# Kernel optimization log

Measured on AMD Instinct MI355X. Metric: run time of the kernel, lower is better.

## Reference

```python
import jax, jax.numpy as jnp
import numpy as np

DIM = 128
K = 4
B, H, W = 2, 256, 256
DEFORM_WEIGHT = 0.3


def conv2d(x, w, b, pad):
    # x [B,C,H,W], w [O,I,kh,kw], stride 1
    y = jax.lax.conv_general_dilated(
        x, w, (1, 1), [(pad, pad), (pad, pad)],
        dimension_numbers=('NCHW', 'OIHW', 'NCHW'))
    return y + b[None, :, None, None]


def gelu(x):
    return jax.nn.gelu(x, approximate=False)  # torch nn.GELU default (erf)


def grid_sample_k(feat, grid):
    """Bilinear grid_sample, padding_mode='border', align_corners=True.
    feat: [B,C,H,W]; grid: [B,K,H,W,2] (x,y) in [-1,1]. Returns [B,C,K,H,W]."""
    Bn, C, Hh, Ww = feat.shape
    px = (grid[..., 0] + 1.0) * 0.5 * (Ww - 1)
    py = (grid[..., 1] + 1.0) * 0.5 * (Hh - 1)
    px = jnp.clip(px, 0.0, Ww - 1)
    py = jnp.clip(py, 0.0, Hh - 1)
    x0 = jnp.floor(px).astype(jnp.int32)
    y0 = jnp.floor(py).astype(jnp.int32)
    x1 = jnp.minimum(x0 + 1, Ww - 1)
    y1 = jnp.minimum(y0 + 1, Hh - 1)
    wx = (px - x0)[:, None]  # [B,1,K,H,W]
    wy = (py - y0)[:, None]
    featf = feat.reshape(Bn, C, Hh * Ww)

    def gather(yi, xi):
        idx = (yi * Ww + xi).reshape(Bn, -1)  # [B, K*H*W]
        g = jax.vmap(lambda f, i: f[:, i])(featf, idx)  # [B,C,K*H*W]
        return g.reshape(Bn, C, *yi.shape[1:])

    v00 = gather(y0, x0)
    v01 = gather(y0, x1)
    v10 = gather(y1, x0)
    v11 = gather(y1, x1)
    return (v00 * (1 - wx) * (1 - wy) + v01 * wx * (1 - wy)
            + v10 * (1 - wx) * wy + v11 * wx * wy)


def setup_inputs() -> dict:
    key = jax.random.key(0)
    ks = jax.random.split(key, 16)
    nrm = lambda k, shape, s: jax.random.normal(k, shape, dtype=jnp.float32) * s
    return {
        'query_feat': jax.random.normal(ks[0], (B, DIM, H, W), dtype=jnp.float32),
        'key_feat': jax.random.normal(ks[1], (B, DIM, H, W), dtype=jnp.float32),
        # offset_net: Conv(dim,dim,3) -> GELU -> Conv(dim,2K,3); small scale keeps offsets sane
        'ow1': nrm(ks[2], (DIM, DIM, 3, 3), 0.02), 'ob1': jnp.zeros((DIM,), jnp.float32),
        'ow2': nrm(ks[3], (2 * K, DIM, 3, 3), 0.01), 'ob2': jnp.zeros((2 * K,), jnp.float32),
        # weight_net: Conv(dim,dim//4,3) -> GELU -> Conv(dim//4,K,1)
        'ww1': nrm(ks[4], (DIM // 4, DIM, 3, 3), 0.05), 'wb1': jnp.zeros((DIM // 4,), jnp.float32),
        'ww2': nrm(ks[5], (K, DIM // 4, 1, 1), 0.05), 'wb2': jnp.zeros((K,), jnp.float32),
        # fusion_conv: Conv(dim,dim,1) -> GELU -> Conv(dim,dim,1)
        'fw1': nrm(ks[6], (DIM, DIM, 1, 1), 0.05), 'fb1': jnp.zeros((DIM,), jnp.float32),
        'fw2': nrm(ks[7], (DIM, DIM, 1, 1), 0.05), 'fb2': jnp.zeros((DIM,), jnp.float32),
    }


def reference(query_feat, key_feat, ow1, ob1, ow2, ob2, ww1, wb1, ww2, wb2,
              fw1, fb1, fw2, fb2):
    offsets = conv2d(gelu(conv2d(query_feat, ow1, ob1, 1)), ow2, ob2, 1)  # [B,2K,H,W]
    wlog = conv2d(gelu(conv2d(query_feat, ww1, wb1, 1)), ww2, wb2, 0)     # [B,K,H,W]
    Bn, C, Hh, Ww = key_feat.shape
    Kp = wlog.shape[1]
    off = offsets.reshape(Bn, Kp, 2, Hh, Ww).transpose(0, 1, 3, 4, 2)  # [B,K,H,W,2]
    gy, gx = jnp.meshgrid(jnp.linspace(-1.0, 1.0, Hh),
                          jnp.linspace(-1.0, 1.0, Ww), indexing='ij')
    base = jnp.stack([gx, gy], axis=-1).astype(off.dtype)  # [H,W,2] (x,y)
    scale = jnp.array([Ww / 2.0, Hh / 2.0], dtype=off.dtype)
    grid = jnp.clip(base + off / scale, -1.0, 1.0)  # [B,K,H,W,2]
    sampled = grid_sample_k(key_feat, grid)  # [B,C,K,H,W]
    wsoft = jax.nn.softmax(wlog, axis=1)[:, None]  # [B,1,K,H,W]
    agg = (sampled * wsoft).sum(axis=2)  # [B,C,H,W]
    fused = conv2d(gelu(conv2d(agg, fw1, fb1, 0)), fw2, fb2, 0)
    return query_feat + fused * DEFORM_WEIGHT
```

## Files before the change

kernel.cpp:

```cpp
#include <hip/hip_runtime.h>
#include <hip/hip_fp16.h>

typedef unsigned short u16;
typedef __attribute__((ext_vector_type(8))) short bf16x8;
typedef __attribute__((ext_vector_type(4))) float f32x4;

constexpr int B_ = 2, C_ = 128, H_ = 256, W_ = 256, P_ = H_ * W_;
constexpr int HP_ = 258, WP_ = 258;

union HU { __half2 h; unsigned int u; };

__device__ __forceinline__ float bf2f(u16 u) {
  union { unsigned int i; float f; } v; v.i = ((unsigned int)u) << 16; return v.f;
}
__device__ __forceinline__ u16 f2bf(float f) {
  union { float f; unsigned int i; } v; v.f = f;
  return (u16)((v.i + 0x7fffu + ((v.i >> 16) & 1u)) >> 16);
}
__device__ __forceinline__ float gelu_f(float x) {
  float u = x * (1.5957691216057308f + 0.071354816272f * x * x);
  return x / (1.0f + __expf(-u));
}

__device__ __forceinline__ void async16(const u16* g, u16* l) {
  __builtin_amdgcn_global_load_lds(
      (const __attribute__((address_space(1))) unsigned int*)g,
      (__attribute__((address_space(3))) unsigned int*)l, 16, 0, 0);
}

__global__ __launch_bounds__(256) void prologue(
    const float* __restrict__ q, const float* __restrict__ key,
    const float* __restrict__ ow1, const float* __restrict__ ow2,
    const float* __restrict__ ww1, const float* __restrict__ fw1,
    const float* __restrict__ fw2,
    u16* __restrict__ qpad, u16* __restrict__ keyn, u16* __restrict__ t1pad,
    u16* __restrict__ wb) {
  __shared__ u16 l[64 * 66];
  const int id = blockIdx.x, tid = threadIdx.x;
  if (id < 8192) {
    int z = id >> 10, r = id & 1023;
    int bx = r & 3, by = r >> 2;
    const float* in; u16* out; int OW, opad;
    if (z < 4) { in = q; out = qpad; OW = WP_; opad = 1; }
    else { z -= 4; in = key; out = keyn; OW = W_; opad = 0; }
    int b = z >> 1, c0 = (z & 1) * 64;
    int h = by, w0 = bx * 64;
    for (int it = 0; it < 4; ++it) {
      int lin = it * 256 + tid;
      int c = lin >> 4, w4 = (lin & 15) * 4;
      float4 v = *(const float4*)&in[(((size_t)b * C_ + c0 + c) * H_ + h) * W_ + w0 + w4];
      l[c * 66 + w4 + 0] = f2bf(v.x);
      l[c * 66 + w4 + 1] = f2bf(v.y);
      l[c * 66 + w4 + 2] = f2bf(v.z);
      l[c * 66 + w4 + 3] = f2bf(v.w);
    }
    __syncthreads();
    int OH = (opad ? HP_ : H_);
    for (int it = 0; it < 16; ++it) {
      int lin = it * 256 + tid;
      int w = lin >> 6, c = lin & 63;
      out[(((size_t)b * OH + h + opad) * OW + (w0 + w + opad)) * C_ + c0 + c] = l[c * 66 + w];
    }
  } else if (id < 10256) {
    int j = id - 8192;
    u16* buf = (j < 1032) ? qpad : t1pad;
    int idx = ((j < 1032) ? j : j - 1032) * 256 + tid;
    int c = idx & 127;
    int t = idx >> 7;
    int pos = t % 258;
    int side = (t / 258) & 3;
    int b = t / (258 * 4);
    int h, w;
    if (side == 0) { h = 0; w = pos; }
    else if (side == 1) { h = 257; w = pos; }
    else if (side == 2) { h = pos; w = 0; }
    else { h = pos; w = 257; }
    buf[(((size_t)b * HP_ + h) * WP_ + w) * C_ + c] = 0;
  } else {
    int idx = (id - 10256) * 256 + tid;
    float v;
    if (idx < 184320) {
      int e = idx & 7, lr = (idx >> 3) & 15, kb = (idx >> 7) & 3;
      int t = idx >> 9;
      int g = t % 10, u = t / 10;
      int cq = u & 3, tap = u >> 2;
      int ci = cq * 32 + kb * 8 + e, co = g * 16 + lr;
      v = (co < 128) ? ow1[(co * 128 + ci) * 9 + tap]
                     : ww1[((co - 128) * 128 + ci) * 9 + tap];
    } else if (idx < 202752) {
      int j = idx - 184320;
      int e = j & 7, lr = (j >> 3) & 15, kb = (j >> 7) & 3;
      int cq = (j >> 9) & 3, tap = j >> 11;
      int ci = cq * 32 + kb * 8 + e, co = lr;
      v = (co < 8) ? ow2[(co * 128 + ci) * 9 + tap] : 0.0f;
    } else if (idx < 219136) {
      v = fw1[idx - 202752];
    } else {
      v = fw2[idx - 219136];
    }
    wb[idx] = f2bf(v);
  }
}

__global__ __launch_bounds__(512, 4) void conv3_big(
    const u16* __restrict__ A, const u16* __restrict__ Wf,
    const float* __restrict__ bias1, const float* __restrict__ bias2,
    u16* __restrict__ outb, u16* __restrict__ outw) {
  constexpr int RPX = 36, ROWU = RPX * 32;
  __shared__ __align__(16) u16 As[6 * ROWU];
  const int tid = threadIdx.x, lane = tid & 63, wave = tid >> 6;
  const int id = blockIdx.x;
  const int s = id >> 3;
  const int h0 = (((id & 7) << 3) | (s & 7)) << 2;
  const int w0 = ((s >> 3) & 7) << 5;
  const int b = s >> 6;
  const int wr = wave >> 1, wc = wave & 1;
  const int wn = wc * 80;
  const int lr = lane & 15, kq = lane >> 4;
  const int gbase = wn >> 4;

  int preA[2][3];
#pragma unroll
  for (int i = 0; i < 2; i++)
#pragma unroll
    for (int kx = 0; kx < 3; kx++) {
      int pxv = i * 16 + lr + kx;
      preA[i][kx] = (pxv * 4 + (kq ^ ((pxv >> 1) & 3))) * 8;
    }

  f32x4 acc[2][5];
#pragma unroll
  for (int i = 0; i < 2; i++)
#pragma unroll
    for (int j = 0; j < 5; j++) { f32x4 z = {0.f, 0.f, 0.f, 0.f}; acc[i][j] = z; }

  for (int cq = 0; cq < 4; ++cq) {
    const int ci0 = cq * 32;
    __syncthreads();
    for (int i = tid; i < 864; i += 512) {
      int ry = i / 144;
      int rem = i - ry * 144;
      int px = rem >> 2, c8 = rem & 3;
      int g = c8 ^ ((px >> 1) & 3);
      async16(A + ((size_t)(b * HP_ + h0 + ry) * WP_ + (w0 + px)) * 128 + ci0 + g * 8,
              As + i * 8);
    }
    __syncthreads();
#pragma unroll
    for (int tap = 0; tap < 9; ++tap) {
      const int ky = tap / 3, kx = tap % 3;
      bf16x8 bfr[5], af[2];
#pragma unroll
      for (int j = 0; j < 5; ++j)
        bfr[j] = *(const bf16x8*)&Wf[(size_t)((((tap * 4 + cq) * 10 + gbase + j) * 4 + kq) * 16 + lr) * 8];
#pragma unroll
      for (int i = 0; i < 2; ++i)
        af[i] = *(const bf16x8*)&As[(wr + ky) * ROWU + preA[i][kx]];
#pragma unroll
      for (int i = 0; i < 2; i++)
#pragma unroll
        for (int j = 0; j < 5; j++)
          acc[i][j] = __builtin_amdgcn_mfma_f32_16x16x32_bf16(af[i], bfr[j], acc[i][j], 0, 0, 0);
    }
  }

  const int h = h0 + wr;
#pragma unroll
  for (int i = 0; i < 2; i++) {
#pragma unroll
    for (int j = 0; j < 5; j++) {
      const int co = wn + j * 16 + lr;
#pragma unroll
      for (int r = 0; r < 4; r++) {
        const int w = w0 + i * 16 + kq * 4 + r;
        float v = acc[i][j][r];
        if (co < 128) {
          v = gelu_f(v + bias1[co]);
          outb[(((size_t)b * HP_ + h + 1) * WP_ + (w + 1)) * 128 + co] = f2bf(v);
        } else {
          v = gelu_f(v + bias2[co - 128]);
          outw[((size_t)b * P_ + (size_t)h * W_ + w) * 32 + (co - 128)] = f2bf(v);
        }
      }
    }
  }
}

__global__ __launch_bounds__(256) void conv_off(
    const u16* __restrict__ A, const u16* __restrict__ Wf,
    const float* __restrict__ bias,
    const u16* __restrict__ w1b, const float* __restrict__ ww2,
    const float* __restrict__ wb2, uint4* __restrict__ desc) {
  constexpr int RPX = 66, ROWU = RPX * 32;
  __shared__ __align__(16) u16 As[6 * ROWU];
  float* off_lds = (float*)As;
  const int tid = threadIdx.x, lane = tid & 63, wave = tid >> 6;
  const int id = blockIdx.x;
  const int s = id >> 3;
  const int h0 = (((id & 7) << 3) | (s & 7)) << 2;
  const int w0 = ((s >> 3) & 3) << 6;
  const int b = s >> 5;
  const int lr = lane & 15, kq = lane >> 4;

  int preA[4][3];
#pragma unroll
  for (int i = 0; i < 4; i++)
#pragma unroll
    for (int kx = 0; kx < 3; kx++) {
      int pxv = i * 16 + lr + kx;
      preA[i][kx] = (pxv * 4 + (kq ^ ((pxv >> 1) & 3))) * 8;
    }

  f32x4 acc[4];
#pragma unroll
  for (int i = 0; i < 4; i++) { f32x4 z = {0.f, 0.f, 0.f, 0.f}; acc[i] = z; }

  for (int cq = 0; cq < 4; ++cq) {
    const int ci0 = cq * 32;
    __syncthreads();
    for (int i = tid; i < 1584; i += 256) {
      int ry = i / 264;
      int rem = i - ry * 264;
      int px = rem >> 2, c8 = rem & 3;
      int g = c8 ^ ((px >> 1) & 3);
      async16(A + ((size_t)(b * HP_ + h0 + ry) * WP_ + (w0 + px)) * 128 + ci0 + g * 8,
              As + i * 8);
    }
    __syncthreads();
#pragma unroll
    for (int tap = 0; tap < 9; ++tap) {
      const int ky = tap / 3, kx = tap % 3;
      bf16x8 bw = *(const bf16x8*)&Wf[(size_t)(((tap * 4 + cq) * 4 + kq) * 16 + lr) * 8];
      bf16x8 af[4];
#pragma unroll
      for (int i = 0; i < 4; ++i)
        af[i] = *(const bf16x8*)&As[(wave + ky) * ROWU + preA[i][kx]];
#pragma unroll
      for (int i = 0; i < 4; i++)
        acc[i] = __builtin_amdgcn_mfma_f32_16x16x32_bf16(af[i], bw, acc[i], 0, 0, 0);
    }
  }

  __syncthreads();
#pragma unroll
  for (int i = 0; i < 4; i++) {
#pragma unroll
    for (int r = 0; r < 4; r++) {
      if (lr < 8) {
        int px = i * 16 + (lane >> 4) * 4 + r;
        off_lds[(wave * 64 + px) * 9 + lr] = acc[i][r] + bias[lr];
      }
    }
  }
  __syncthreads();

  const int pp = tid;
  const int h = h0 + (pp >> 6), w = w0 + (pp & 63);
  const int pix = b * P_ + h * W_ + w;
  const u16* wp = w1b + (size_t)pix * 32;
  float f[32];
#pragma unroll
  for (int i = 0; i < 32; i += 2) {
    unsigned u = *(const unsigned*)&wp[i];
    f[i] = bf2f((u16)u); f[i + 1] = bf2f((u16)(u >> 16));
  }
  float lg[4];
#pragma unroll
  for (int k = 0; k < 4; k++) {
    float sacc = wb2[k];
#pragma unroll
    for (int i = 0; i < 32; i++) sacc = fmaf(ww2[k * 32 + i], f[i], sacc);
    lg[k] = sacc;
  }
  float mx = fmaxf(fmaxf(lg[0], lg[1]), fmaxf(lg[2], lg[3]));
  float e[4], sum = 0.f;
#pragma unroll
  for (int k = 0; k < 4; k++) { e[k] = __expf(lg[k] - mx); sum += e[k]; }
  const float inv = 1.0f / sum;
#pragma unroll
  for (int k = 0; k < 4; k++) {
    float ox = off_lds[pp * 9 + 2 * k], oy = off_lds[pp * 9 + 2 * k + 1];
    float gx = (2.0f * w / 255.0f - 1.0f) + ox * (1.0f / 128.0f);
    float gy = (2.0f * h / 255.0f - 1.0f) + oy * (1.0f / 128.0f);
    gx = fminf(fmaxf(gx, -1.f), 1.f);
    gy = fminf(fmaxf(gy, -1.f), 1.f);
    float px = fminf(fmaxf((gx + 1.f) * 127.5f, 0.f), 255.f);
    float py = fminf(fmaxf((gy + 1.f) * 127.5f, 0.f), 255.f);
    int x0 = (int)px, y0 = (int)py;
    int x1 = min(x0 + 1, 255), y1 = min(y0 + 1, 255);
    float wx = px - x0, wy = py - y0;
    float wk = e[k] * inv;
    float w00 = (1.f - wx) * (1.f - wy) * wk, w01 = wx * (1.f - wy) * wk;
    float w10 = (1.f - wx) * wy * wk,         w11 = wx * wy * wk;
    HU t01, t23;
    t01.h = __floats2half2_rn(w00, w01);
    t23.h = __floats2half2_rn(w10, w11);
    uint4 d;
    d.x = (unsigned)(y0 * 256 + x0) | ((unsigned)(x1 - x0) << 16) | ((unsigned)(y1 - y0) << 17);
    d.y = t01.u; d.z = t23.u; d.w = 0;
    desc[(size_t)pix * 4 + k] = d;
  }
}

__global__ __launch_bounds__(256) void sampler(
    const uint4* __restrict__ desc, const u16* __restrict__ keyn, u16* __restrict__ agg) {
  const int tid = threadIdx.x, lane = tid & 63, wv = tid >> 6;
  const int pix = blockIdx.x * 4 + wv;
  const int b = pix >> 16;
  const u16* kb = keyn + (size_t)b * (P_ * C_) + 2 * lane;
  float a0 = 0.f, a1 = 0.f;
#pragma unroll
  for (int k = 0; k < 4; ++k) {
    uint4 d = desc[(size_t)pix * 4 + k];
    const int boff = (int)(d.x & 0xFFFFu) << 7;
    const int o01 = (int)((d.x >> 16) & 1u) << 7;
    const int o10 = (int)((d.x >> 17) & 1u) << 15;
    const u16* c0 = kb + boff;
    unsigned u00 = *(const unsigned*)(c0);
    unsigned u01 = *(const unsigned*)(c0 + o01);
    unsigned u10 = *(const unsigned*)(c0 + o10);
    unsigned u11 = *(const unsigned*)(c0 + o10 + o01);
    HU t01, t23; t01.u = d.y; t23.u = d.z;
    float2 wA = __half22float2(t01.h);
    float2 wB = __half22float2(t23.h);
    a0 = fmaf(wA.x, bf2f((u16)u00), a0);
    a0 = fmaf(wA.y, bf2f((u16)u01), a0);
    a0 = fmaf(wB.x, bf2f((u16)u10), a0);
    a0 = fmaf(wB.y, bf2f((u16)u11), a0);
    a1 = fmaf(wA.x, bf2f((u16)(u00 >> 16)), a1);
    a1 = fmaf(wA.y, bf2f((u16)(u01 >> 16)), a1);
    a1 = fmaf(wB.x, bf2f((u16)(u10 >> 16)), a1);
    a1 = fmaf(wB.y, bf2f((u16)(u11 >> 16)), a1);
  }
  unsigned outu = ((unsigned)f2bf(a1) << 16) | (unsigned)f2bf(a0);
  *(unsigned*)&agg[(size_t)pix * C_ + 2 * lane] = outu;
}

__global__ __launch_bounds__(512, 4) void conv_fuse(
    const u16* __restrict__ Aagg, const u16* __restrict__ W1, const u16* __restrict__ W2,
    const float* __restrict__ b1, const float* __restrict__ b2,
    const float* __restrict__ resid, float* __restrict__ out) {
  __shared__ __align__(16) u16 SM[16384];
  __shared__ __align__(16) u16 T2[128 * 136];
  u16* As = SM;
  u16* Bs = SM + 8192;
  const int tid = threadIdx.x, lane = tid & 63, wave = tid >> 6;
  const int h = blockIdx.y, w0 = blockIdx.x * 128;
  const int b = blockIdx.z;
  const int wr = wave >> 1, wc = wave & 1;
  const int wm = wr * 32, wn = wc * 64;
  const int lr = lane & 15, kq = lane >> 4;
  const int sw = lr & 7;

  f32x4 acc[2][4];
#pragma unroll
  for (int i = 0; i < 2; i++)
#pragma unroll
    for (int j = 0; j < 4; j++) { f32x4 z = {0.f, 0.f, 0.f, 0.f}; acc[i][j] = z; }

  for (int c = 0; c < 2; ++c) {
    const int ci0 = c << 6;
    const u16* Ab = Aagg + (((size_t)b * H_ + h) * W_ + w0) * 128 + ci0;
    const u16* Wb = W1 + ci0;
    __syncthreads();
    for (int i = tid; i < 128 * 8; i += 512) {
      int r = i >> 3, cb = i & 7;
      async16(Ab + r * 128 + ((cb ^ (r & 7)) << 3), As + i * 8);
    }
    for (int i = tid; i < 128 * 8; i += 512) {
      int r = i >> 3, cb = i & 7;
      async16(Wb + r * 128 + ((cb ^ (r & 7)) << 3), Bs + i * 8);
    }
    __syncthreads();
#pragma unroll
    for (int ks = 0; ks < 2; ++ks) {
      const int kb = ks * 4 + kq;
      bf16x8 af[2], bfr[4];
#pragma unroll
      for (int i = 0; i < 2; i++)
        af[i] = *(const bf16x8*)&As[(wm + i * 16 + lr) * 64 + ((kb ^ sw) << 3)];
#pragma unroll
      for (int j = 0; j < 4; j++)
        bfr[j] = *(const bf16x8*)&Bs[(wn + j * 16 + lr) * 64 + ((kb ^ sw) << 3)];
#pragma unroll
      for (int i = 0; i < 2; i++)
#pragma unroll
        for (int j = 0; j < 4; j++)
          acc[i][j] = __builtin_amdgcn_mfma_f32_16x16x32_bf16(af[i], bfr[j], acc[i][j], 0, 0, 0);
    }
  }

#pragma unroll
  for (int i = 0; i < 2; i++)
#pragma unroll
    for (int j = 0; j < 4; j++) {
      const int co = wn + j * 16 + lr;
#pragma unroll
      for (int r = 0; r < 4; r++) {
        const int px = wm + i * 16 + kq * 4 + r;
        T2[px * 136 + co] = f2bf(gelu_f(acc[i][j][r] + b1[co]));
      }
    }
  __syncthreads();
  for (int i = tid; i < 2048; i += 512) {
    int r = i >> 4, sl = i & 15;
    int g = sl ^ (r & 7);
    async16(W2 + r * 128 + g * 8, SM + i * 8);
  }
  __syncthreads();

#pragma unroll
  for (int i = 0; i < 2; i++)
#pragma unroll
    for (int j = 0; j < 4; j++) { f32x4 z = {0.f, 0.f, 0.f, 0.f}; acc[i][j] = z; }
#pragma unroll
  for (int ks = 0; ks < 4; ++ks) {
    const int kc = ks * 4 + kq;
    bf16x8 af[2], bfr[4];
#pragma unroll
    for (int i = 0; i < 2; i++)
      af[i] = *(const bf16x8*)&T2[(wm + i * 16 + lr) * 136 + kc * 8];
#pragma unroll
    for (int j = 0; j < 4; j++) {
      int rr = wn + j * 16 + lr;
      bfr[j] = *(const bf16x8*)&SM[rr * 128 + (kc ^ (rr & 7)) * 8];
    }
#pragma unroll
    for (int i = 0; i < 2; i++)
#pragma unroll
      for (int j = 0; j < 4; j++)
        acc[i][j] = __builtin_amdgcn_mfma_f32_16x16x32_bf16(af[i], bfr[j], acc[i][j], 0, 0, 0);
  }

#pragma unroll
  for (int i = 0; i < 2; i++) {
#pragma unroll
    for (int j = 0; j < 4; j++) {
      const int co = wn + j * 16 + lr;
      const int w = w0 + wm + i * 16 + kq * 4;
      size_t idx = ((size_t)b * 128 + co) * (size_t)P_ + (size_t)h * W_ + w;
      float4 rv = *(const float4*)&resid[idx];
      float bi = b2[co];
      float4 ov;
      ov.x = rv.x + 0.3f * (acc[i][j][0] + bi);
      ov.y = rv.y + 0.3f * (acc[i][j][1] + bi);
      ov.z = rv.z + 0.3f * (acc[i][j][2] + bi);
      ov.w = rv.w + 0.3f * (acc[i][j][3] + bi);
      *(float4*)&out[idx] = ov;
    }
  }
}

extern "C" void kernel_launch(void* const* d_in, const int* in_sizes, int n_in,
                              void* d_out, int out_size, void* d_ws, size_t ws_size,
                              hipStream_t stream) {
  (void)in_sizes; (void)n_in; (void)out_size; (void)ws_size;
  const float* q   = (const float*)d_in[0];
  const float* key = (const float*)d_in[1];
  const float* ow1 = (const float*)d_in[2];
  const float* ob1 = (const float*)d_in[3];
  const float* ow2 = (const float*)d_in[4];
  const float* ob2 = (const float*)d_in[5];
  const float* ww1 = (const float*)d_in[6];
  const float* wb1 = (const float*)d_in[7];
  const float* ww2 = (const float*)d_in[8];
  const float* wb2 = (const float*)d_in[9];
  const float* fw1 = (const float*)d_in[10];
  const float* fb1 = (const float*)d_in[11];
  const float* fw2 = (const float*)d_in[12];
  const float* fb2 = (const float*)d_in[13];
  float* out = (float*)d_out;
  char* ws = (char*)d_ws;

  u16* qpad  = (u16*)(ws);
  u16* t1pad = (u16*)(ws + 34080768);
  u16* keyn  = (u16*)(ws + 68161536);
  u16* w1b   = (u16*)(ws + 101715968);
  u16* wbuf  = (u16*)(ws + 110104576);
  uint4* desc = (uint4*)ws;
  u16* agg = t1pad;

  prologue<<<11176, 256, 0, stream>>>(q, key, ow1, ow2, ww1, fw1, fw2,
                                      qpad, keyn, t1pad, wbuf);
  conv3_big<<<1024, 512, 0, stream>>>(qpad, wbuf, ob1, wb1, t1pad, w1b);
  conv_off<<<512, 256, 0, stream>>>(t1pad, wbuf + 184320, ob2, w1b, ww2, wb2, desc);
  sampler<<<32768, 256, 0, stream>>>(desc, keyn, agg);
  conv_fuse<<<dim3(2, 256, 2), 512, 0, stream>>>(agg, wbuf + 202752, wbuf + 219136,
                                                 fb1, fb2, q, out);
}
```

Before: 357.0 us.

## Fuse bilinear sampler into the 1x1 conv fuse kernel via shared memory

Merges the separate sampler kernel into the fusion-conv kernel. Each workgroup gathers its 128 pixels' aggregated features straight into a swizzled LDS tile, which removes the global write and re-read of the agg tensor and one kernel launch. Shared memory buffers are reassigned: the W1 slice is staged in T2, and the W2 load now overlaps the GELU epilogue. The trade-off is that the gather runs inside a kernel with fewer blocks and limited occupancy, so latency hiding for the random key reads may be weaker.

```diff
diff --git a/kernel.cpp b/kernel.cpp
--- a/kernel.cpp
+++ b/kernel.cpp
@@ -302,48 +302,13 @@
   }
 }
 
-__global__ __launch_bounds__(256) void sampler(
-    const uint4* __restrict__ desc, const u16* __restrict__ keyn, u16* __restrict__ agg) {
-  const int tid = threadIdx.x, lane = tid & 63, wv = tid >> 6;
-  const int pix = blockIdx.x * 4 + wv;
-  const int b = pix >> 16;
-  const u16* kb = keyn + (size_t)b * (P_ * C_) + 2 * lane;
-  float a0 = 0.f, a1 = 0.f;
-#pragma unroll
-  for (int k = 0; k < 4; ++k) {
-    uint4 d = desc[(size_t)pix * 4 + k];
-    const int boff = (int)(d.x & 0xFFFFu) << 7;
-    const int o01 = (int)((d.x >> 16) & 1u) << 7;
-    const int o10 = (int)((d.x >> 17) & 1u) << 15;
-    const u16* c0 = kb + boff;
-    unsigned u00 = *(const unsigned*)(c0);
-    unsigned u01 = *(const unsigned*)(c0 + o01);
-    unsigned u10 = *(const unsigned*)(c0 + o10);
-    unsigned u11 = *(const unsigned*)(c0 + o10 + o01);
-    HU t01, t23; t01.u = d.y; t23.u = d.z;
-    float2 wA = __half22float2(t01.h);
-    float2 wB = __half22float2(t23.h);
-    a0 = fmaf(wA.x, bf2f((u16)u00), a0);
-    a0 = fmaf(wA.y, bf2f((u16)u01), a0);
-    a0 = fmaf(wB.x, bf2f((u16)u10), a0);
-    a0 = fmaf(wB.y, bf2f((u16)u11), a0);
-    a1 = fmaf(wA.x, bf2f((u16)(u00 >> 16)), a1);
-    a1 = fmaf(wA.y, bf2f((u16)(u01 >> 16)), a1);
-    a1 = fmaf(wB.x, bf2f((u16)(u10 >> 16)), a1);
-    a1 = fmaf(wB.y, bf2f((u16)(u11 >> 16)), a1);
-  }
-  unsigned outu = ((unsigned)f2bf(a1) << 16) | (unsigned)f2bf(a0);
-  *(unsigned*)&agg[(size_t)pix * C_ + 2 * lane] = outu;
-}
-
-__global__ __launch_bounds__(512, 4) void conv_fuse(
-    const u16* __restrict__ Aagg, const u16* __restrict__ W1, const u16* __restrict__ W2,
+__global__ __launch_bounds__(512, 4) void sample_fuse(
+    const uint4* __restrict__ desc, const u16* __restrict__ keyn,
+    const u16* __restrict__ W1, const u16* __restrict__ W2,
     const float* __restrict__ b1, const float* __restrict__ b2,
     const float* __restrict__ resid, float* __restrict__ out) {
-  __shared__ __align__(16) u16 SM[16384];
+  __shared__ __align__(16) u16 SM[128 * 128];
   __shared__ __align__(16) u16 T2[128 * 136];
-  u16* As = SM;
-  u16* Bs = SM + 8192;
   const int tid = threadIdx.x, lane = tid & 63, wave = tid >> 6;
   const int h = blockIdx.y, w0 = blockIdx.x * 128;
   const int b = blockIdx.z;
@@ -352,6 +317,45 @@
   const int lr = lane & 15, kq = lane >> 4;
   const int sw = lr & 7;
 
+  {
+    const u16* kb = keyn + (size_t)b * (P_ * C_) + 2 * lane;
+    const int pxbase = wave * 16;
+    const size_t pixbase = (size_t)b * P_ + (size_t)h * W_ + w0 + pxbase;
+    const int half64 = (lane >> 5) * 64;
+    const int gg = (lane >> 2) & 7;
+    const int e2 = (lane & 3) * 2;
+    for (int p = 0; p < 16; ++p) {
+      const size_t pix = pixbase + p;
+      float a0 = 0.f, a1 = 0.f;
+#pragma unroll
+      for (int k = 0; k < 4; ++k) {
+        uint4 d = desc[pix * 4 + k];
+        const int boff = (int)(d.x & 0xFFFFu) << 7;
+        const int o01 = (int)((d.x >> 16) & 1u) << 7;
+        const int o10 = (int)((d.x >> 17) & 1u) << 15;
+        const u16* c0 = kb + boff;
+        unsigned u00 = *(const unsigned*)(c0);
+        unsigned u01 = *(const unsigned*)(c0 + o01);
+        unsigned u10 = *(const unsigned*)(c0 + o10);
+        unsigned u11 = *(const unsigned*)(c0 + o10 + o01);
+        HU t01, t23; t01.u = d.y; t23.u = d.z;
+        float2 wA = __half22float2(t01.h);
+        float2 wB = __half22float2(t23.h);
+        a0 = fmaf(wA.x, bf2f((u16)u00), a0);
+        a0 = fmaf(wA.y, bf2f((u16)u01), a0);
+        a0 = fmaf(wB.x, bf2f((u16)u10), a0);
+        a0 = fmaf(wB.y, bf2f((u16)u11), a0);
+        a1 = fmaf(wA.x, bf2f((u16)(u00 >> 16)), a1);
+        a1 = fmaf(wA.y, bf2f((u16)(u01 >> 16)), a1);
+        a1 = fmaf(wB.x, bf2f((u16)(u10 >> 16)), a1);
+        a1 = fmaf(wB.y, bf2f((u16)(u11 >> 16)), a1);
+      }
+      const int px = pxbase + p;
+      unsigned outu = ((unsigned)f2bf(a1) << 16) | (unsigned)f2bf(a0);
+      *(unsigned*)&SM[px * 128 + half64 + ((gg ^ (px & 7)) << 3) + e2] = outu;
+    }
+  }
+
   f32x4 acc[2][4];
 #pragma unroll
   for (int i = 0; i < 2; i++)
@@ -360,16 +364,11 @@
 
   for (int c = 0; c < 2; ++c) {
     const int ci0 = c << 6;
-    const u16* Ab = Aagg + (((size_t)b * H_ + h) * W_ + w0) * 128 + ci0;
     const u16* Wb = W1 + ci0;
     __syncthreads();
-    for (int i = tid; i < 128 * 8; i += 512) {
+    for (int i = tid; i < 1024; i += 512) {
       int r = i >> 3, cb = i & 7;
-      async16(Ab + r * 128 + ((cb ^ (r & 7)) << 3), As + i * 8);
-    }
-    for (int i = tid; i < 128 * 8; i += 512) {
-      int r = i >> 3, cb = i & 7;
-      async16(Wb + r * 128 + ((cb ^ (r & 7)) << 3), Bs + i * 8);
+      async16(Wb + r * 128 + ((cb ^ (r & 7)) << 3), T2 + i * 8);
     }
     __syncthreads();
 #pragma unroll
@@ -378,10 +377,10 @@
       bf16x8 af[2], bfr[4];
 #pragma unroll
       for (int i = 0; i < 2; i++)
-        af[i] = *(const bf16x8*)&As[(wm + i * 16 + lr) * 64 + ((kb ^ sw) << 3)];
+        af[i] = *(const bf16x8*)&SM[(wm + i * 16 + lr) * 128 + ci0 + ((kb ^ sw) << 3)];
 #pragma unroll
       for (int j = 0; j < 4; j++)
-        bfr[j] = *(const bf16x8*)&Bs[(wn + j * 16 + lr) * 64 + ((kb ^ sw) << 3)];
+        bfr[j] = *(const bf16x8*)&T2[(wn + j * 16 + lr) * 64 + ((kb ^ sw) << 3)];
 #pragma unroll
       for (int i = 0; i < 2; i++)
 #pragma unroll
@@ -389,7 +388,13 @@
           acc[i][j] = __builtin_amdgcn_mfma_f32_16x16x32_bf16(af[i], bfr[j], acc[i][j], 0, 0, 0);
     }
   }
-
+  __syncthreads();
+
+  for (int i = tid; i < 2048; i += 512) {
+    int r = i >> 4, sl = i & 15;
+    int g = sl ^ (r & 7);
+    async16(W2 + r * 128 + g * 8, SM + i * 8);
+  }
 #pragma unroll
   for (int i = 0; i < 2; i++)
 #pragma unroll
@@ -401,12 +406,6 @@
         T2[px * 136 + co] = f2bf(gelu_f(acc[i][j][r] + b1[co]));
       }
     }
-  __syncthreads();
-  for (int i = tid; i < 2048; i += 512) {
-    int r = i >> 4, sl = i & 15;
-    int g = sl ^ (r & 7);
-    async16(W2 + r * 128 + g * 8, SM + i * 8);
-  }
   __syncthreads();
 
 #pragma unroll
@@ -478,13 +477,11 @@
   u16* w1b   = (u16*)(ws + 101715968);
   u16* wbuf  = (u16*)(ws + 110104576);
   uint4* desc = (uint4*)ws;
-  u16* agg = t1pad;
 
   prologue<<<11176, 256, 0, stream>>>(q, key, ow1, ow2, ww1, fw1, fw2,
                                       qpad, keyn, t1pad, wbuf);
   conv3_big<<<1024, 512, 0, stream>>>(qpad, wbuf, ob1, wb1, t1pad, w1b);
   conv_off<<<512, 256, 0, stream>>>(t1pad, wbuf + 184320, ob2, w1b, ww2, wb2, desc);
-  sampler<<<32768, 256, 0, stream>>>(desc, keyn, agg);
-  conv_fuse<<<dim3(2, 256, 2), 512, 0, stream>>>(agg, wbuf + 202752, wbuf + 219136,
-                                                 fb1, fb2, q, out);
-}
+  sample_fuse<<<dim3(2, 256, 2), 512, 0, stream>>>(desc, keyn, wbuf + 202752,
+                                                   wbuf + 219136, fb1, fb2, q, out);
+}
```

Result: no change. 356.6 us (-0.1%).
